# Kernel optimization log

Measured on AMD Instinct MI355X. Metric: run time of the kernel, lower is better.

## Reference

```python
import jax, jax.numpy as jnp
import numpy as np

B, L, E, H, D = 4, 4096, 1024, 16, 64  # batch, seq, embed, heads, head_dim
EPS = 1e-6


def setup_inputs() -> dict:
    key = jax.random.key(0)
    k1, k2, k3 = jax.random.split(key, 3)
    return {
        "q": jax.random.normal(k1, (B, L, E), dtype=jnp.float32),
        "k": jax.random.normal(k2, (B, L, E), dtype=jnp.float32),
        "v": jax.random.normal(k3, (B, L, E), dtype=jnp.float32),
        "mask": jnp.ones((B, L), dtype=jnp.float32),
    }


def _split_heads(x):
    # (B, L, E) -> (B*H, L, D)
    return x.reshape(B, L, H, D).transpose(0, 2, 1, 3).reshape(B * H, L, D)


def reference(q, k, v, mask):
    # feature map: relu
    q = jax.nn.relu(q)
    k = jax.nn.relu(k)
    # padding mask applied to keys/values
    k = k * mask[:, :, None]
    v = v * mask[:, :, None]
    q = _split_heads(q)
    k = _split_heads(k)
    v = _split_heads(v)
    # cosFormer sin/cos reweighting: pi/2 * i / m for i = 1..L
    idx = (np.pi / 2) * jnp.arange(1, L + 1, dtype=jnp.float32) / L
    s = jnp.sin(idx)[None, :, None]  # (1, L, 1)
    c = jnp.cos(idx)[None, :, None]
    q_ = jnp.concatenate([q * s, q * c], axis=-1)  # (B*H, L, 2D)
    k_ = jnp.concatenate([k * s, k * c], axis=-1)
    # linear-attention KV accumulation (non-causal): (B*H, 2D, D)
    kv = jnp.einsum('nld,nlm->ndm', k_, v)
    # normalizer
    z = 1.0 / jnp.maximum(jnp.einsum('nld,nd->nl', q_, k_.sum(axis=1)), EPS)
    out = jnp.einsum('nld,ndm,nl->nlm', q_, kv, z)  # (B*H, L, D)
    return out.reshape(B, H, L, D)
```

## Files before the change

### kernel.cpp

```cpp
#include <hip/hip_runtime.h>
#include <hip/hip_bf16.h>
#include <math.h>

#define B_ 4
#define L_ 4096
#define E_ 1024
#define H_ 16
#define D_ 64
#define N_ 64
#define D2_ 128
#define EPS_ 1e-6f

#define CH_ 16
#define LC_ (L_ / CH_)
#define LT_ 64
#define NST_ (LC_ / LT_)

#define DANG_ 3.83495197e-4f

typedef short short8 __attribute__((ext_vector_type(8)));
typedef float f32x4 __attribute__((ext_vector_type(4)));
typedef unsigned int u32;
typedef unsigned short u16;

static __device__ __forceinline__ u32 pack2bf(float a, float b) {
  union { __hip_bfloat16 h; u16 s; } x, y;
  x.h = __float2bfloat16(a);
  y.h = __float2bfloat16(b);
  return (u32)x.s | ((u32)y.s << 16);
}

static __device__ __forceinline__ short bf1(float a) {
  union { __hip_bfloat16 h; short s; } x;
  x.h = __float2bfloat16(a);
  return x.s;
}

static __device__ __forceinline__ void gld16(const void* g, void* l) {
  __builtin_amdgcn_global_load_lds(
      (const __attribute__((address_space(1))) unsigned int*)g,
      (__attribute__((address_space(3))) unsigned int*)l, 16, 0, 0);
}

__global__ __launch_bounds__(256, 2) void phase1_mfma(
    const float* __restrict__ k, const float* __restrict__ v,
    const float* __restrict__ mask,
    float* __restrict__ part_kv, float* __restrict__ part_ks) {
  __shared__ __align__(16) u16 ka[2][D2_ * 72];
  __shared__ __align__(16) u16 vt[2][D_ * 72];

  const int bid = blockIdx.x;
  const int n = bid & 63;
  const int ch = bid >> 6;
  const int b = n >> 4;
  const int h = n & 15;
  const int t = threadIdx.x;
  const int wv = t >> 6;
  const int lane = t & 63;
  const int c_lo = lane & 15;
  const int lp = lane >> 4;
  const int c = wv * 16 + c_lo;

  f32x4 acc[2][4];
#pragma unroll
  for (int i = 0; i < 2; ++i)
#pragma unroll
    for (int j = 0; j < 4; ++j) acc[i][j] = (f32x4)0.f;
  float kss = 0.f, ksc = 0.f;

  const int l0 = ch * LC_;
  const size_t gb0 = (size_t)(b * L_ + l0) * E_ + h * 64 + c;

  float Ak0[8], Ak1[8], Av0[8], Av1[8], Am;
  float Bk0[8], Bk1[8], Bv0[8], Bv1[8], Bm;

#define P1_PREF(Rk0, Rk1, Rv0, Rv1, Rm, S)                                   \
  do {                                                                       \
    const size_t gs_ = gb0 + (size_t)(S) * (LT_ * E_);                       \
    _Pragma("unroll") for (int i_ = 0; i_ < 8; ++i_) {                       \
      const size_t g0_ = gs_ + (size_t)(8 * i_ + 2 * lp) * E_;               \
      Rk0[i_] = k[g0_];                                                      \
      Rk1[i_] = k[g0_ + E_];                                                 \
      Rv0[i_] = v[g0_];                                                      \
      Rv1[i_] = v[g0_ + E_];                                                 \
    }                                                                        \
    Rm = mask[(size_t)b * L_ + l0 + (S) * LT_ + lane];                       \
  } while (0)

#define P1_STAGE(Rk0, Rk1, Rv0, Rv1, Rm, S, BUF)                             \
  do {                                                                       \
    const int lb_ = l0 + (S) * LT_;                                          \
    _Pragma("unroll") for (int i_ = 0; i_ < 8; ++i_) {                       \
      const int l_ = 8 * i_ + 2 * lp;                                        \
      const float m0_ = __shfl(Rm, l_);                                      \
      const float m1_ = __shfl(Rm, l_ + 1);                                  \
      float s0_, c0_, s1_, c1_;                                              \
      __sincosf((float)(lb_ + l_ + 1) * DANG_, &s0_, &c0_);                  \
      __sincosf((float)(lb_ + l_ + 2) * DANG_, &s1_, &c1_);                  \
      const float kr0_ = fmaxf(Rk0[i_], 0.f) * m0_;                          \
      const float kr1_ = fmaxf(Rk1[i_], 0.f) * m1_;                          \
      const float ks0_ = kr0_ * s0_, ks1_ = kr1_ * s1_;                      \
      const float kc0_ = kr0_ * c0_, kc1_ = kr1_ * c1_;                      \
      const int li_ = 4 * i_ + lp;                                           \
      ((u32*)ka[BUF])[c * 36 + li_] = pack2bf(ks0_, ks1_);                   \
      ((u32*)ka[BUF])[(c + 64) * 36 + li_] = pack2bf(kc0_, kc1_);            \
      ((u32*)vt[BUF])[c * 36 + li_] = pack2bf(Rv0[i_] * m0_, Rv1[i_] * m1_); \
      kss += ks0_ + ks1_;                                                    \
      ksc += kc0_ + kc1_;                                                    \
    }                                                                        \
  } while (0)

#define P1_MMA(BUF)                                                          \
  do {                                                                       \
    _Pragma("unroll") for (int kk_ = 0; kk_ < 2; ++kk_) {                    \
      const int colo_ = kk_ * 32 + lp * 8;                                   \
      short8 af_[2], bf_[4];                                                 \
      _Pragma("unroll") for (int dt_ = 0; dt_ < 2; ++dt_)                    \
          af_[dt_] = *(const short8*)                                        \
              &ka[BUF][(wv * 32 + dt_ * 16 + c_lo) * 72 + colo_];            \
      _Pragma("unroll") for (int mt_ = 0; mt_ < 4; ++mt_)                    \
          bf_[mt_] = *(const short8*)                                        \
              &vt[BUF][(mt_ * 16 + c_lo) * 72 + colo_];                      \
      _Pragma("unroll") for (int dt_ = 0; dt_ < 2; ++dt_)                    \
          _Pragma("unroll") for (int mt_ = 0; mt_ < 4; ++mt_)                \
              acc[dt_][mt_] = __builtin_amdgcn_mfma_f32_16x16x32_bf16(       \
                  af_[dt_], bf_[mt_], acc[dt_][mt_], 0, 0, 0);               \
    }                                                                        \
  } while (0)

  P1_PREF(Ak0, Ak1, Av0, Av1, Am, 0);
  P1_STAGE(Ak0, Ak1, Av0, Av1, Am, 0, 0);
  if (2 < NST_) P1_PREF(Ak0, Ak1, Av0, Av1, Am, 2);
  P1_PREF(Bk0, Bk1, Bv0, Bv1, Bm, 1);
  __syncthreads();

#pragma unroll
  for (int st = 0; st < NST_; st += 2) {
    if (st + 1 < NST_) {
      P1_STAGE(Bk0, Bk1, Bv0, Bv1, Bm, st + 1, 1);
      if (st + 3 < NST_) P1_PREF(Bk0, Bk1, Bv0, Bv1, Bm, st + 3);
    }
    P1_MMA(0);
    __syncthreads();
    if (st + 1 < NST_) {
      if (st + 2 < NST_) {
        P1_STAGE(Ak0, Ak1, Av0, Av1, Am, st + 2, 0);
        if (st + 4 < NST_) P1_PREF(Ak0, Ak1, Av0, Av1, Am, st + 4);
      }
      P1_MMA(1);
      __syncthreads();
    }
  }

  const size_t pbase = (size_t)(ch * N_ + n) * (D2_ * D_);
#pragma unroll
  for (int dt = 0; dt < 2; ++dt) {
    const int d = wv * 32 + dt * 16 + lp * 4;
#pragma unroll
    for (int mt = 0; mt < 4; ++mt) {
      const int mcol = mt * 16 + c_lo;
#pragma unroll
      for (int r = 0; r < 4; ++r)
        part_kv[pbase + (size_t)(d + r) * D_ + mcol] = acc[dt][mt][r];
    }
  }
  kss += __shfl_xor(kss, 16); kss += __shfl_xor(kss, 32);
  ksc += __shfl_xor(ksc, 16); ksc += __shfl_xor(ksc, 32);
  if (lp == 0) {
    part_ks[(size_t)(ch * N_ + n) * D2_ + c] = kss;
    part_ks[(size_t)(ch * N_ + n) * D2_ + c + 64] = ksc;
  }
}

__global__ __launch_bounds__(256) void reduce_t(
    const float* __restrict__ part_kv, const float* __restrict__ part_ks,
    u16* __restrict__ kvt, float* __restrict__ ks) {
  __shared__ __align__(16) float tsh[16 * 68];
  const int bid = blockIdx.x;
  const int n = bid >> 3;
  const int sl = bid & 7;
  const int t = threadIdx.x;

  const int e0 = sl * 1024 + t * 4;
  f32x4 s = (f32x4)0.f;
#pragma unroll
  for (int cc = 0; cc < CH_; ++cc)
    s += *(const f32x4*)&part_kv[(size_t)(cc * N_ + n) * (D2_ * D_) + e0];
  *(f32x4*)&tsh[(t >> 4) * 68 + (t & 15) * 4] = s;

  if (sl == 0 && t < D2_) {
    float ss = 0.f;
#pragma unroll
    for (int cc = 0; cc < CH_; ++cc)
      ss += part_ks[(size_t)(cc * N_ + n) * D2_ + t];
    ks[n * D2_ + t] = ss;
  }
  __syncthreads();

  const int m = t >> 2;
  const int d4 = (t & 3) * 4;
  const u32 lo = pack2bf(tsh[(d4 + 0) * 68 + m], tsh[(d4 + 1) * 68 + m]);
  const u32 hi = pack2bf(tsh[(d4 + 2) * 68 + m], tsh[(d4 + 3) * 68 + m]);
  uint2 pk; pk.x = lo; pk.y = hi;
  *(uint2*)&kvt[(size_t)n * (D2_ * D_) + (size_t)m * D2_ + sl * 16 + d4] = pk;
}

__global__ __launch_bounds__(256, 3) void phase2_mfma(
    const float* __restrict__ q, const u16* __restrict__ kvt,
    const float* __restrict__ ks, float* __restrict__ out) {
  __shared__ __align__(16) float qsh[2 * 64 * 64];
  __shared__ __align__(16) u16 kbsh[64 * 128];

  const int bid = blockIdx.x;
  const int n = bid & 63;
  const int g2 = bid >> 6;
  const int b = n >> 4, h = n & 15;
  const int t = threadIdx.x;
  const int wv = t >> 6, lane = t & 63;
  const int c_lo = lane & 15, quad = lane >> 4;
  const int l0 = g2 * 128;

  const float* qbase = q + (size_t)(b * L_ + l0) * E_ + h * 64;
  const u16* kvbase = kvt + (size_t)n * (D2_ * D_);
  const int rsub = lane >> 4;
  const int g = lane & 15;
#pragma unroll
  for (int j = 0; j < 4; ++j) {
    const int r = wv * 16 + j * 4 + rsub;
    const int sw = (g ^ (r & 15));
    gld16(kvbase + (size_t)r * D2_ + (sw << 3),
          kbsh + (wv * 16 + j * 4) * 128);
    gld16(qbase + (size_t)r * E_ + (sw << 2),
          qsh + (wv * 16 + j * 4) * 64);
    gld16(qbase + (size_t)(64 + r) * E_ + (sw << 2),
          qsh + 4096 + (wv * 16 + j * 4) * 64);
  }

  const float* ksn = ks + n * D2_;
  short8 bks[4];
#pragma unroll
  for (int kk = 0; kk < 4; ++kk) {
    const f32x4 ka_ = *(const f32x4*)(ksn + kk * 32 + quad * 8);
    const f32x4 kb_ = *(const f32x4*)(ksn + kk * 32 + quad * 8 + 4);
    short8 tt = {0, 0, 0, 0, 0, 0, 0, 0};
    if (c_lo == 0) {
#pragma unroll
      for (int j = 0; j < 4; ++j) {
        tt[j] = bf1(ka_[j]);
        tt[j + 4] = bf1(kb_[j]);
      }
    }
    bks[kk] = tt;
  }

  __syncthreads();

#pragma unroll
  for (int cc = 0; cc < 2; ++cc) {
    const int row = wv * 16 + c_lo;
    const int glr = l0 + cc * 64 + row;
    float sv, cv;
    __sincosf((float)(glr + 1) * DANG_, &sv, &cv);

    const float* qrow = qsh + cc * 4096 + row * 64;
    const int sw = row & 15;
    const f32x4 a0 = *(const f32x4*)(qrow + (((2 * quad) ^ sw) << 2));
    const f32x4 a1 = *(const f32x4*)(qrow + (((2 * quad + 1) ^ sw) << 2));
    const f32x4 a2 = *(const f32x4*)(qrow + (((8 + 2 * quad) ^ sw) << 2));
    const f32x4 a3 = *(const f32x4*)(qrow + (((9 + 2 * quad) ^ sw) << 2));

    short8 af[4];
#pragma unroll
    for (int j = 0; j < 4; ++j) {
      const float x0 = fmaxf(a0[j], 0.f);
      const float x1 = fmaxf(a1[j], 0.f);
      const float x2 = fmaxf(a2[j], 0.f);
      const float x3 = fmaxf(a3[j], 0.f);
      af[0][j] = bf1(x0 * sv); af[0][j + 4] = bf1(x1 * sv);
      af[1][j] = bf1(x2 * sv); af[1][j + 4] = bf1(x3 * sv);
      af[2][j] = bf1(x0 * cv); af[2][j + 4] = bf1(x1 * cv);
      af[3][j] = bf1(x2 * cv); af[3][j + 4] = bf1(x3 * cv);
    }

    f32x4 acc[4];
#pragma unroll
    for (int mt = 0; mt < 4; ++mt) acc[mt] = (f32x4)0.f;
    f32x4 acc5 = (f32x4)0.f;

#pragma unroll
    for (int kk = 0; kk < 4; ++kk) {
#pragma unroll
      for (int mt = 0; mt < 4; ++mt) {
        const int m = mt * 16 + c_lo;
        const short8 bfr = *(const short8*)
            &kbsh[m * 128 + (((kk * 4 + quad) ^ (m & 15)) << 3)];
        acc[mt] =
            __builtin_amdgcn_mfma_f32_16x16x32_bf16(af[kk], bfr, acc[mt], 0, 0, 0);
      }
      acc5 = __builtin_amdgcn_mfma_f32_16x16x32_bf16(af[kk], bks[kk], acc5, 0, 0, 0);
    }

#pragma unroll
    for (int r = 0; r < 4; ++r) {
      const float den = __shfl(acc5[r], quad * 16);
      const float z = 1.f / fmaxf(den, EPS_);
      const int gl = l0 + cc * 64 + wv * 16 + quad * 4 + r;
      const size_t ob = (size_t)n * (L_ * D_) + (size_t)gl * D_;
#pragma unroll
      for (int mt = 0; mt < 4; ++mt)
        out[ob + mt * 16 + c_lo] = acc[mt][r] * z;
    }
  }
}

extern "C" void kernel_launch(void* const* d_in, const int* in_sizes, int n_in,
                              void* d_out, int out_size, void* d_ws,
                              size_t ws_size, hipStream_t stream) {
  const float* q = (const float*)d_in[0];
  const float* k = (const float*)d_in[1];
  const float* v = (const float*)d_in[2];
  const float* mask = (const float*)d_in[3];
  float* out = (float*)d_out;

  float* part_kv = (float*)d_ws;
  float* part_ks = part_kv + (size_t)CH_ * N_ * D2_ * D_;
  u16* kvt = (u16*)(part_ks + (size_t)CH_ * N_ * D2_);
  float* ks = (float*)(kvt + (size_t)N_ * D2_ * D_);

  phase1_mfma<<<dim3(CH_ * N_), dim3(256), 0, stream>>>(k, v, mask, part_kv, part_ks);
  reduce_t<<<dim3(N_ * 8), dim3(256), 0, stream>>>(part_kv, part_ks, kvt, ks);
  phase2_mfma<<<dim3(N_ * 32), dim3(256), 0, stream>>>(q, kvt, ks, out);
}
```

Before: 251.5 us.

## Stream K/V tiles via async global-to-LDS loads and compute key sums with MFMA

```diff
diff --git a/kernel.cpp b/kernel.cpp
--- a/kernel.cpp
+++ b/kernel.cpp
@@ -13,8 +13,8 @@
 
 #define CH_ 16
 #define LC_ (L_ / CH_)
-#define LT_ 64
-#define NST_ (LC_ / LT_)
+#define LT2_ 32
+#define NST_ (LC_ / LT2_)
 
 #define DANG_ 3.83495197e-4f
 
@@ -42,12 +42,32 @@
       (__attribute__((address_space(3))) unsigned int*)l, 16, 0, 0);
 }
 
-__global__ __launch_bounds__(256, 2) void phase1_mfma(
+#define BAR_() __builtin_amdgcn_s_barrier()
+#define WAIT_LGKM0_()                                     \
+  {                                                       \
+    asm volatile("s_waitcnt lgkmcnt(0)" ::: "memory");    \
+    __builtin_amdgcn_sched_barrier(0);                    \
+  }
+#define WAIT_VM4_()                                       \
+  {                                                       \
+    asm volatile("s_waitcnt vmcnt(4)" ::: "memory");      \
+    __builtin_amdgcn_sched_barrier(0);                    \
+  }
+#define WAIT_VM0_()                                       \
+  {                                                       \
+    asm volatile("s_waitcnt vmcnt(0)" ::: "memory");      \
+    __builtin_amdgcn_sched_barrier(0);                    \
+  }
+
+__global__ __launch_bounds__(256, 3) void phase1_mfma(
     const float* __restrict__ k, const float* __restrict__ v,
     const float* __restrict__ mask,
     float* __restrict__ part_kv, float* __restrict__ part_ks) {
-  __shared__ __align__(16) u16 ka[2][D2_ * 72];
-  __shared__ __align__(16) u16 vt[2][D_ * 72];
+  __shared__ __align__(16) float kraw[2][LT2_ * 64];
+  __shared__ __align__(16) float vraw[2][LT2_ * 64];
+  __shared__ __align__(16) u16 ka[D2_ * 40];
+  __shared__ __align__(16) u16 vt[D_ * 40];
+  __shared__ float msh[LC_];
 
   const int bid = blockIdx.x;
   const int n = bid & 63;
@@ -59,98 +79,116 @@
   const int lane = t & 63;
   const int c_lo = lane & 15;
   const int lp = lane >> 4;
-  const int c = wv * 16 + c_lo;
+  const int lp2 = t >> 4;
+  const int dg = t & 15;
+  const int l0 = ch * LC_;
+
+  u32* ka32 = (u32*)ka;
+  u32* vt32 = (u32*)vt;
 
   f32x4 acc[2][4];
 #pragma unroll
   for (int i = 0; i < 2; ++i)
 #pragma unroll
     for (int j = 0; j < 4; ++j) acc[i][j] = (f32x4)0.f;
-  float kss = 0.f, ksc = 0.f;
-
-  const int l0 = ch * LC_;
-  const size_t gb0 = (size_t)(b * L_ + l0) * E_ + h * 64 + c;
-
-  float Ak0[8], Ak1[8], Av0[8], Av1[8], Am;
-  float Bk0[8], Bk1[8], Bv0[8], Bv1[8], Bm;
-
-#define P1_PREF(Rk0, Rk1, Rv0, Rv1, Rm, S)                                   \
+  f32x4 acc5[2];
+  acc5[0] = (f32x4)0.f;
+  acc5[1] = (f32x4)0.f;
+
+  short8 bones = {0, 0, 0, 0, 0, 0, 0, 0};
+  if (c_lo == 0) {
+#pragma unroll
+    for (int j = 0; j < 8; ++j) bones[j] = (short)0x3F80;
+  }
+
+#define P1_GLD(S, BUF)                                                       \
   do {                                                                       \
-    const size_t gs_ = gb0 + (size_t)(S) * (LT_ * E_);                       \
-    _Pragma("unroll") for (int i_ = 0; i_ < 8; ++i_) {                       \
-      const size_t g0_ = gs_ + (size_t)(8 * i_ + 2 * lp) * E_;               \
-      Rk0[i_] = k[g0_];                                                      \
-      Rk1[i_] = k[g0_ + E_];                                                 \
-      Rv0[i_] = v[g0_];                                                      \
-      Rv1[i_] = v[g0_ + E_];                                                 \
-    }                                                                        \
-    Rm = mask[(size_t)b * L_ + l0 + (S) * LT_ + lane];                       \
-  } while (0)
-
-#define P1_STAGE(Rk0, Rk1, Rv0, Rv1, Rm, S, BUF)                             \
-  do {                                                                       \
-    const int lb_ = l0 + (S) * LT_;                                          \
-    _Pragma("unroll") for (int i_ = 0; i_ < 8; ++i_) {                       \
-      const int l_ = 8 * i_ + 2 * lp;                                        \
-      const float m0_ = __shfl(Rm, l_);                                      \
-      const float m1_ = __shfl(Rm, l_ + 1);                                  \
-      float s0_, c0_, s1_, c1_;                                              \
-      __sincosf((float)(lb_ + l_ + 1) * DANG_, &s0_, &c0_);                  \
-      __sincosf((float)(lb_ + l_ + 2) * DANG_, &s1_, &c1_);                  \
-      const float kr0_ = fmaxf(Rk0[i_], 0.f) * m0_;                          \
-      const float kr1_ = fmaxf(Rk1[i_], 0.f) * m1_;                          \
-      const float ks0_ = kr0_ * s0_, ks1_ = kr1_ * s1_;                      \
-      const float kc0_ = kr0_ * c0_, kc1_ = kr1_ * c1_;                      \
-      const int li_ = 4 * i_ + lp;                                           \
-      ((u32*)ka[BUF])[c * 36 + li_] = pack2bf(ks0_, ks1_);                   \
-      ((u32*)ka[BUF])[(c + 64) * 36 + li_] = pack2bf(kc0_, kc1_);            \
-      ((u32*)vt[BUF])[c * 36 + li_] = pack2bf(Rv0[i_] * m0_, Rv1[i_] * m1_); \
-      kss += ks0_ + ks1_;                                                    \
-      ksc += kc0_ + kc1_;                                                    \
+    _Pragma("unroll") for (int j_ = 0; j_ < 2; ++j_) {                       \
+      const int r32_ = 8 * wv + 4 * j_ + lp;                                 \
+      const int lg_ = l0 + (S) * LT2_ + r32_;                                \
+      const size_t gs_ = (size_t)(b * L_ + lg_) * E_ + h * 64;               \
+      const int so_ = (c_lo ^ (r32_ & 15)) << 2;                             \
+      gld16(k + gs_ + so_, &kraw[BUF][(8 * wv + 4 * j_) * 64]);              \
+      gld16(v + gs_ + so_, &vraw[BUF][(8 * wv + 4 * j_) * 64]);              \
     }                                                                        \
   } while (0)
 
-#define P1_MMA(BUF)                                                          \
+#define P1_PACK(BUF, S)                                                      \
   do {                                                                       \
-    _Pragma("unroll") for (int kk_ = 0; kk_ < 2; ++kk_) {                    \
-      const int colo_ = kk_ * 32 + lp * 8;                                   \
-      short8 af_[2], bf_[4];                                                 \
-      _Pragma("unroll") for (int dt_ = 0; dt_ < 2; ++dt_)                    \
-          af_[dt_] = *(const short8*)                                        \
-              &ka[BUF][(wv * 32 + dt_ * 16 + c_lo) * 72 + colo_];            \
-      _Pragma("unroll") for (int mt_ = 0; mt_ < 4; ++mt_)                    \
-          bf_[mt_] = *(const short8*)                                        \
-              &vt[BUF][(mt_ * 16 + c_lo) * 72 + colo_];                      \
-      _Pragma("unroll") for (int dt_ = 0; dt_ < 2; ++dt_)                    \
-          _Pragma("unroll") for (int mt_ = 0; mt_ < 4; ++mt_)                \
-              acc[dt_][mt_] = __builtin_amdgcn_mfma_f32_16x16x32_bf16(       \
-                  af_[dt_], bf_[mt_], acc[dt_][mt_], 0, 0, 0);               \
+    const int la_ = 2 * lp2, lb_ = la_ + 1;                                  \
+    const float m0_ = msh[(S) * LT2_ + la_];                                 \
+    const float m1_ = msh[(S) * LT2_ + lb_];                                 \
+    const int lga_ = l0 + (S) * LT2_ + la_;                                  \
+    float s0_, c0_, s1_, c1_;                                                \
+    __sincosf((float)(lga_ + 1) * DANG_, &s0_, &c0_);                        \
+    __sincosf((float)(lga_ + 2) * DANG_, &s1_, &c1_);                        \
+    const int sa_ = la_ & 15, sb_ = lb_ & 15;                                \
+    _Pragma("unroll") for (int dj_ = 0; dj_ < 4; ++dj_) {                    \
+      const int d_ = dg + 16 * dj_;                                          \
+      const int gl_ = d_ >> 2, su_ = d_ & 3;                                 \
+      const float k0_ = kraw[BUF][la_ * 64 + ((gl_ ^ sa_) << 2) + su_];      \
+      const float k1_ = kraw[BUF][lb_ * 64 + ((gl_ ^ sb_) << 2) + su_];      \
+      const float v0_ = vraw[BUF][la_ * 64 + ((gl_ ^ sa_) << 2) + su_];      \
+      const float v1_ = vraw[BUF][lb_ * 64 + ((gl_ ^ sb_) << 2) + su_];      \
+      const float kr0_ = fmaxf(k0_, 0.f) * m0_;                              \
+      const float kr1_ = fmaxf(k1_, 0.f) * m1_;                              \
+      ka32[d_ * 20 + lp2] = pack2bf(kr0_ * s0_, kr1_ * s1_);                 \
+      ka32[(d_ + 64) * 20 + lp2] = pack2bf(kr0_ * c0_, kr1_ * c1_);          \
+      vt32[d_ * 20 + lp2] = pack2bf(v0_ * m0_, v1_ * m1_);                   \
     }                                                                        \
   } while (0)
 
-  P1_PREF(Ak0, Ak1, Av0, Av1, Am, 0);
-  P1_STAGE(Ak0, Ak1, Av0, Av1, Am, 0, 0);
-  if (2 < NST_) P1_PREF(Ak0, Ak1, Av0, Av1, Am, 2);
-  P1_PREF(Bk0, Bk1, Bv0, Bv1, Bm, 1);
-  __syncthreads();
-
-#pragma unroll
-  for (int st = 0; st < NST_; st += 2) {
-    if (st + 1 < NST_) {
-      P1_STAGE(Bk0, Bk1, Bv0, Bv1, Bm, st + 1, 1);
-      if (st + 3 < NST_) P1_PREF(Bk0, Bk1, Bv0, Bv1, Bm, st + 3);
-    }
-    P1_MMA(0);
-    __syncthreads();
-    if (st + 1 < NST_) {
-      if (st + 2 < NST_) {
-        P1_STAGE(Ak0, Ak1, Av0, Av1, Am, st + 2, 0);
-        if (st + 4 < NST_) P1_PREF(Ak0, Ak1, Av0, Av1, Am, st + 4);
-      }
-      P1_MMA(1);
-      __syncthreads();
-    }
-  }
+#define P1_MMA()                                                             \
+  do {                                                                       \
+    short8 af_[2], bf_[4];                                                   \
+    _Pragma("unroll") for (int dt_ = 0; dt_ < 2; ++dt_)                      \
+        af_[dt_] = *(const short8*)&ka[(wv * 32 + dt_ * 16 + c_lo) * 40 +    \
+                                       lp * 8];                              \
+    _Pragma("unroll") for (int mt_ = 0; mt_ < 4; ++mt_)                      \
+        bf_[mt_] = *(const short8*)&vt[(mt_ * 16 + c_lo) * 40 + lp * 8];     \
+    _Pragma("unroll") for (int dt_ = 0; dt_ < 2; ++dt_) {                    \
+      _Pragma("unroll") for (int mt_ = 0; mt_ < 4; ++mt_)                    \
+          acc[dt_][mt_] = __builtin_amdgcn_mfma_f32_16x16x32_bf16(           \
+              af_[dt_], bf_[mt_], acc[dt_][mt_], 0, 0, 0);                   \
+      acc5[dt_] = __builtin_amdgcn_mfma_f32_16x16x32_bf16(af_[dt_], bones,   \
+                                                          acc5[dt_], 0, 0,   \
+                                                          0);                \
+    }                                                                        \
+  } while (0)
+
+#define P1_STEP(S, BUF)                                                      \
+  do {                                                                       \
+    P1_PACK(BUF, S);                                                         \
+    WAIT_LGKM0_();                                                           \
+    BAR_();                                                                  \
+    P1_MMA();                                                                \
+    P1_GLD((S) + 2, BUF);                                                    \
+    WAIT_VM4_();                                                             \
+    BAR_();                                                                  \
+  } while (0)
+
+  if (wv == 0) gld16(mask + (size_t)b * L_ + l0 + lane * 4, msh);
+  P1_GLD(0, 0);
+  P1_GLD(1, 1);
+  WAIT_VM4_();
+  BAR_();
+
+  P1_STEP(0, 0);
+  P1_STEP(1, 1);
+  P1_STEP(2, 0);
+  P1_STEP(3, 1);
+  P1_STEP(4, 0);
+  P1_STEP(5, 1);
+  P1_PACK(0, 6);
+  WAIT_LGKM0_();
+  BAR_();
+  P1_MMA();
+  WAIT_VM0_();
+  BAR_();
+  P1_PACK(1, 7);
+  WAIT_LGKM0_();
+  BAR_();
+  P1_MMA();
 
   const size_t pbase = (size_t)(ch * N_ + n) * (D2_ * D_);
 #pragma unroll
@@ -164,11 +202,13 @@
         part_kv[pbase + (size_t)(d + r) * D_ + mcol] = acc[dt][mt][r];
     }
   }
-  kss += __shfl_xor(kss, 16); kss += __shfl_xor(kss, 32);
-  ksc += __shfl_xor(ksc, 16); ksc += __shfl_xor(ksc, 32);
-  if (lp == 0) {
-    part_ks[(size_t)(ch * N_ + n) * D2_ + c] = kss;
-    part_ks[(size_t)(ch * N_ + n) * D2_ + c + 64] = ksc;
+  if (c_lo == 0) {
+#pragma unroll
+    for (int dt = 0; dt < 2; ++dt)
+#pragma unroll
+      for (int r = 0; r < 4; ++r)
+        part_ks[(size_t)(ch * N_ + n) * D2_ + wv * 32 + dt * 16 + lp * 4 + r] =
+            acc5[dt][r];
   }
 }
 
```

After: 247.0 us. About the same (-1.8%).
